# Performance work log

Measured on AMD Instinct MI355X. Metric: run time of the kernel, lower is better.

The kernel has to match this reference:

```python
import jax, jax.numpy as jnp
import numpy as np

D_MODEL = 1024
N_HEAD = 16
HEAD_DIM = D_MODEL // N_HEAD


def setup_inputs() -> dict:
    key = jax.random.key(0)
    k1, k2, k3 = jax.random.split(key, 3)
    B, T = 2, 2048
    x = jax.random.normal(k1, (B, T, D_MODEL), dtype=jnp.float32)
    # nn.MultiheadAttention packed in-projection: (3*D, D), xavier-like scale
    w_in = jax.random.normal(k2, (3 * D_MODEL, D_MODEL), dtype=jnp.float32) * (1.0 / np.sqrt(D_MODEL))
    b_in = jnp.zeros((3 * D_MODEL,), dtype=jnp.float32)
    w_out = jax.random.normal(k3, (D_MODEL, D_MODEL), dtype=jnp.float32) * (1.0 / np.sqrt(D_MODEL))
    b_out = jnp.zeros((D_MODEL,), dtype=jnp.float32)
    return {"x": x, "w_in": w_in, "b_in": b_in, "w_out": w_out, "b_out": b_out}


def reference(x, w_in, b_in, w_out, b_out):
    B, T, D = x.shape
    H, hd = N_HEAD, HEAD_DIM
    # packed QKV projection (torch Linear convention: y = x @ W.T + b)
    qkv = x @ w_in.T + b_in                      # [B, T, 3D]
    q, k, v = jnp.split(qkv, 3, axis=-1)
    # [B, H, T, hd]
    q = q.reshape(B, T, H, hd).transpose(0, 2, 1, 3)
    k = k.reshape(B, T, H, hd).transpose(0, 2, 1, 3)
    v = v.reshape(B, T, H, hd).transpose(0, 2, 1, 3)
    scale = 1.0 / np.sqrt(hd).astype(np.float32)
    scores = jnp.einsum("bhqd,bhkd->bhqk", q * scale, k)  # [B, H, T, T]
    causal = jnp.tril(jnp.ones((T, T), dtype=bool))
    scores = jnp.where(causal, scores, jnp.finfo(scores.dtype).min)
    attn = jax.nn.softmax(scores, axis=-1)
    ctx = jnp.einsum("bhqk,bhkd->bhqd", attn, v)           # [B, H, T, hd]
    ctx = ctx.transpose(0, 2, 1, 3).reshape(B, T, D)
    return ctx @ w_out.T + b_out
```

## Files before the change

kernel.cpp:

```cpp
#include <hip/hip_runtime.h>


#define T_SEQ 2048
#define D_MODEL 1024
#define NEG_BIG (-1.0e30f)

typedef float f32x4 __attribute__((ext_vector_type(4)));
typedef short s16x8 __attribute__((ext_vector_type(8)));
typedef __bf16 bf16x8 __attribute__((ext_vector_type(8)));

__device__ __forceinline__ f32x4 mfma16(s16x8 a, s16x8 b, f32x4 c) {
    return __builtin_amdgcn_mfma_f32_16x16x32_bf16(
        __builtin_bit_cast(bf16x8, a), __builtin_bit_cast(bf16x8, b), c, 0, 0, 0);
}

__device__ __forceinline__ short f2bf(float f) {
    unsigned int u = __float_as_uint(f);
    u += 0x7fffu + ((u >> 16) & 1u);
    return (short)(u >> 16);
}
__device__ __forceinline__ short f2bf_fast(float f) {
    return (short)((__float_as_uint(f) + 0x8000u) >> 16);
}
__device__ __forceinline__ float bf2f(short s) {
    return __uint_as_float(((unsigned int)(unsigned short)s) << 16);
}

__device__ __forceinline__ void async_lds16(const short* g, short* l) {
    __builtin_amdgcn_global_load_lds(
        (const __attribute__((address_space(1))) unsigned int*)g,
        (__attribute__((address_space(3))) unsigned int*)l, 16, 0, 0);
}

#define N_X   4194304
#define N_WI  3145728
#define N_BI  3072
#define N_WO  1048576
#define N_BO  1024
#define V_X   (N_X  / 4)
#define V_WI  (N_WI / 4)
#define V_BI  (N_BI / 4)
#define V_WO  (N_WO / 4)
#define V_BO  (N_BO / 4)
#define V_TOT (V_X + V_WI + V_BI + V_WO + V_BO)

__global__ __launch_bounds__(256) void canon_all_kernel(
    const float* __restrict__ x, const float* __restrict__ wi,
    const float* __restrict__ bi, const float* __restrict__ wo,
    const float* __restrict__ bo,
    short* __restrict__ xb, short* __restrict__ wib, short* __restrict__ bib,
    short* __restrict__ wob, short* __restrict__ bob)
{
    int i = blockIdx.x * 256 + threadIdx.x;
    if (i >= V_TOT) return;
    const float* src; short* dst; int off;
    if      (i < V_X)                    { src = x;  dst = xb;  off = i; }
    else if (i < V_X+V_WI)               { src = wi; dst = wib; off = i - V_X; }
    else if (i < V_X+V_WI+V_BI)          { src = bi; dst = bib; off = i - V_X - V_WI; }
    else if (i < V_X+V_WI+V_BI+V_WO)     { src = wo; dst = wob; off = i - V_X - V_WI - V_BI; }
    else                                 { src = bo; dst = bob; off = i - V_X - V_WI - V_BI - V_WO; }
    float4 v = ((const float4*)src)[off];
    short4 o = { f2bf(v.x), f2bf(v.y), f2bf(v.z), f2bf(v.w) };
    ((short4*)dst)[off] = o;
}

#define Q_SCALE 0.18033688f

__global__ __launch_bounds__(256) void gemm_qkv_kernel(
    const short* __restrict__ A, const short* __restrict__ B,
    const short* __restrict__ bias,
    short* __restrict__ qo, short* __restrict__ ko, short* __restrict__ vo)
{
    const int K = 1024;
    alignas(16) __shared__ short As[128][32];
    alignas(16) __shared__ short Bs[128][32];
    const int m0 = blockIdx.x * 128;
    const int n0 = blockIdx.y * 128;
    const int tid = threadIdx.x;
    const int lane = tid & 63;
    const int w = tid >> 6;
    const int wm = (w >> 1) * 64, wn = (w & 1) * 64;
    const int quad = lane >> 4, l16 = lane & 15;

    f32x4 acc[4][4];
    const f32x4 zero = {0.f, 0.f, 0.f, 0.f};
#pragma unroll
    for (int i = 0; i < 4; ++i)
#pragma unroll
        for (int j = 0; j < 4; ++j) acc[i][j] = zero;

    const int lrow = lane >> 2;
    const int lcol = (lane & 3) * 8;
    const short* gA0 = &A[(m0 + w*32      + lrow) * K + lcol];
    const short* gA1 = &A[(m0 + w*32 + 16 + lrow) * K + lcol];
    const short* gB0 = &B[(n0 + w*32      + lrow) * K + lcol];
    const short* gB1 = &B[(n0 + w*32 + 16 + lrow) * K + lcol];
    short* lA0 = &As[w*32][0];
    short* lA1 = &As[w*32 + 16][0];
    short* lB0 = &Bs[w*32][0];
    short* lB1 = &Bs[w*32 + 16][0];

    for (int k0 = 0; k0 < K; k0 += 32) {
        __syncthreads();
        async_lds16(gA0 + k0, lA0);
        async_lds16(gA1 + k0, lA1);
        async_lds16(gB0 + k0, lB0);
        async_lds16(gB1 + k0, lB1);
        __syncthreads();

        s16x8 af[4], bfr[4];
#pragma unroll
        for (int i = 0; i < 4; ++i) af[i]  = *(const s16x8*)&As[wm + i*16 + l16][quad*8];
#pragma unroll
        for (int j = 0; j < 4; ++j) bfr[j] = *(const s16x8*)&Bs[wn + j*16 + l16][quad*8];
#pragma unroll
        for (int i = 0; i < 4; ++i)
#pragma unroll
            for (int j = 0; j < 4; ++j)
                acc[i][j] = mfma16(af[i], bfr[j], acc[i][j]);
    }

#pragma unroll
    for (int j = 0; j < 4; ++j) {
        int n = n0 + wn + j*16 + l16;
        float bi = bf2f(bias[n]);
        int which = n >> 10;
        short* dst = (which == 0) ? qo : (which == 1) ? ko : vo;
        float scl = (which == 0) ? Q_SCALE : 1.0f;
        int h = (n >> 6) & 15, d = n & 63;
#pragma unroll
        for (int i = 0; i < 4; ++i) {
#pragma unroll
            for (int r = 0; r < 4; ++r) {
                int m = m0 + wm + i*16 + quad*4 + r;
                int b = m >> 11, t = m & 2047;
                float v = (acc[i][j][r] + bi) * scl;
                dst[(((b*16 + h) * 2048) + t) * 64 + d] = f2bf(v);
            }
        }
    }
}

__global__ __launch_bounds__(256) void attn_kernel(
    const short* __restrict__ Q, const short* __restrict__ K,
    const short* __restrict__ V, short* __restrict__ ctx)
{
    alignas(16) __shared__ short Ks[64][72];
    alignas(16) __shared__ short Vt[64][64];
    alignas(16) __shared__ short Pl[4][16][76];

    const int bh = blockIdx.x;
    const int qt = 31 - (int)blockIdx.y;
    const int qbase = qt * 64;
    const int tid = threadIdx.x;
    const int w = tid >> 6, lane = tid & 63;
    const int quad = lane >> 4, l16 = lane & 15;
    const int b = bh >> 4, h = bh & 15;

    const short* Qb = Q + bh * T_SEQ * 64;
    const short* Kb = K + bh * T_SEQ * 64;
    const short* Vb = V + bh * T_SEQ * 64;

    const short* qrow = Qb + (qbase + w*16 + l16) * 64;
    const s16x8 qa0 = *(const s16x8*)(qrow + quad*8);
    const s16x8 qa1 = *(const s16x8*)(qrow + 32 + quad*8);

    const f32x4 zero = {0.f, 0.f, 0.f, 0.f};
    f32x4 o[4];
#pragma unroll
    for (int dt = 0; dt < 4; ++dt) o[dt] = zero;
    float lrow[4] = {0.f, 0.f, 0.f, 0.f};

    const int sr  = tid >> 3;
    const int scl = (tid & 7) * 8;

    for (int s0 = 0; s0 <= qbase; s0 += 64) {
        __syncthreads();
        *(float4*)&Ks[sr][scl]    = *(const float4*)&Kb[(s0 + sr) * 64 + scl];
        *(float4*)&Ks[sr+32][scl] = *(const float4*)&Kb[(s0 + sr + 32) * 64 + scl];
        float4 v0 = *(const float4*)&Vb[(s0 + sr) * 64 + scl];
        float4 v1 = *(const float4*)&Vb[(s0 + sr + 32) * 64 + scl];
        const short* p0 = (const short*)&v0;
        const short* p1 = (const short*)&v1;
#pragma unroll
        for (int j = 0; j < 8; ++j) {
            Vt[scl + j][sr ^ scl]        = p0[j];
            Vt[scl + j][(sr + 32) ^ scl] = p1[j];
        }
        __syncthreads();

        s16x8 kb0[4], kb1[4];
#pragma unroll
        for (int sub = 0; sub < 4; ++sub) {
            kb0[sub] = *(const s16x8*)&Ks[sub*16 + l16][quad*8];
            kb1[sub] = *(const s16x8*)&Ks[sub*16 + l16][32 + quad*8];
        }

        f32x4 S[4];
#pragma unroll
        for (int sub = 0; sub < 4; ++sub)
            S[sub] = mfma16(qa1, kb1[sub], mfma16(qa0, kb0[sub], zero));

        if (s0 == qbase) {
            int q0 = qbase + w*16 + quad*4;
#pragma unroll
            for (int sub = 0; sub < 4; ++sub) {
                int scg = s0 + sub*16 + l16;
#pragma unroll
                for (int r = 0; r < 4; ++r)
                    if (scg > q0 + r) S[sub][r] = NEG_BIG;
            }
        }

        int prow = quad*4;
#pragma unroll
        for (int sub = 0; sub < 4; ++sub) {
#pragma unroll
            for (int r = 0; r < 4; ++r) {
                float p = exp2f(S[sub][r]);
                lrow[r] += p;
                Pl[w][prow + r][sub*16 + l16] = f2bf_fast(p);
            }
        }

        s16x8 pa0 = *(const s16x8*)&Pl[w][l16][quad*8];
        s16x8 pa1 = *(const s16x8*)&Pl[w][l16][32 + quad*8];
#pragma unroll
        for (int dt = 0; dt < 4; ++dt) {
            int e = (dt*2 + (l16 >> 3)) & 7;
            s16x8 vb0 = *(const s16x8*)&Vt[dt*16 + l16][8 * (quad ^ e)];
            s16x8 vb1 = *(const s16x8*)&Vt[dt*16 + l16][8 * ((quad + 4) ^ e)];
            o[dt] = mfma16(pa1, vb1, mfma16(pa0, vb0, o[dt]));
        }
    }

#pragma unroll
    for (int r = 0; r < 4; ++r) {
        float l = lrow[r];
        l += __shfl_xor(l, 1, 16);
        l += __shfl_xor(l, 2, 16);
        l += __shfl_xor(l, 4, 16);
        l += __shfl_xor(l, 8, 16);
        float inv = 1.0f / l;
        int qg = qbase + w*16 + quad*4 + r;
        int base = (b * T_SEQ + qg) * D_MODEL + h * 64 + l16;
#pragma unroll
        for (int dt = 0; dt < 4; ++dt)
            ctx[base + dt*16] = f2bf(o[dt][r] * inv);
    }
}

__global__ __launch_bounds__(256) void gemm_out_kernel(
    const short* __restrict__ A, const short* __restrict__ B,
    const short* __restrict__ bias, float* __restrict__ out)
{
    const int K = 1024;
    alignas(16) __shared__ short As[128][32];
    alignas(16) __shared__ short Bs[128][32];
    const int m0 = blockIdx.x * 128;
    const int n0 = blockIdx.y * 128;
    const int tid = threadIdx.x;
    const int lane = tid & 63;
    const int w = tid >> 6;
    const int wm = (w >> 1) * 64, wn = (w & 1) * 64;
    const int quad = lane >> 4, l16 = lane & 15;

    f32x4 acc[4][4];
    const f32x4 zero = {0.f, 0.f, 0.f, 0.f};
#pragma unroll
    for (int i = 0; i < 4; ++i)
#pragma unroll
        for (int j = 0; j < 4; ++j) acc[i][j] = zero;

    const int lrow = lane >> 2;
    const int lcol = (lane & 3) * 8;
    const short* gA0 = &A[(m0 + w*32      + lrow) * K + lcol];
    const short* gA1 = &A[(m0 + w*32 + 16 + lrow) * K + lcol];
    const short* gB0 = &B[(n0 + w*32      + lrow) * K + lcol];
    const short* gB1 = &B[(n0 + w*32 + 16 + lrow) * K + lcol];
    short* lA0 = &As[w*32][0];
    short* lA1 = &As[w*32 + 16][0];
    short* lB0 = &Bs[w*32][0];
    short* lB1 = &Bs[w*32 + 16][0];

    for (int k0 = 0; k0 < K; k0 += 32) {
        __syncthreads();
        async_lds16(gA0 + k0, lA0);
        async_lds16(gA1 + k0, lA1);
        async_lds16(gB0 + k0, lB0);
        async_lds16(gB1 + k0, lB1);
        __syncthreads();

        s16x8 af[4], bfr[4];
#pragma unroll
        for (int i = 0; i < 4; ++i) af[i]  = *(const s16x8*)&As[wm + i*16 + l16][quad*8];
#pragma unroll
        for (int j = 0; j < 4; ++j) bfr[j] = *(const s16x8*)&Bs[wn + j*16 + l16][quad*8];
#pragma unroll
        for (int i = 0; i < 4; ++i)
#pragma unroll
            for (int j = 0; j < 4; ++j)
                acc[i][j] = mfma16(af[i], bfr[j], acc[i][j]);
    }

#pragma unroll
    for (int j = 0; j < 4; ++j) {
        int n = n0 + wn + j*16 + l16;
        float bi = bf2f(bias[n]);
#pragma unroll
        for (int i = 0; i < 4; ++i) {
#pragma unroll
            for (int r = 0; r < 4; ++r) {
                int m = m0 + wm + i*16 + quad*4 + r;
                out[m * 1024 + n] = acc[i][j][r] + bi;
            }
        }
    }
}

extern "C" void kernel_launch(void* const* d_in, const int* in_sizes, int n_in,
                              void* d_out, int out_size, void* d_ws, size_t ws_size,
                              hipStream_t stream) {
    float* out = (float*)d_out;
    char* ws = (char*)d_ws;

    const size_t MB = 1u << 20;
    short* xb     = (short*)(ws);
    short* w_inb  = (short*)(ws + 8*MB);
    short* b_inb  = (short*)(ws + 14*MB);
    short* w_outb = (short*)(ws + 15*MB);
    short* b_outb = (short*)(ws + 17*MB);
    short* qb     = (short*)(ws + 18*MB);
    short* kb     = (short*)(ws + 26*MB);
    short* vb     = (short*)(ws + 34*MB);
    short* ctxb   = (short*)(ws + 42*MB);

    canon_all_kernel<<<(V_TOT + 255) / 256, 256, 0, stream>>>(
        (const float*)d_in[0], (const float*)d_in[1], (const float*)d_in[2],
        (const float*)d_in[3], (const float*)d_in[4],
        xb, w_inb, b_inb, w_outb, b_outb);

    gemm_qkv_kernel<<<dim3(32, 24), 256, 0, stream>>>(xb, w_inb, b_inb, qb, kb, vb);
    attn_kernel<<<dim3(32, 32), 256, 0, stream>>>(qb, kb, vb, ctxb);
    gemm_out_kernel<<<dim3(32, 8), 256, 0, stream>>>(ctxb, w_outb, b_outb, out);
}
```

Before: 193.6 us.

## Store V transposed from QKV GEMM, swap attention MFMA operands, narrow out-proj tiles

The QKV GEMM now writes V in a transposed [bh][d][t] layout with packed 4-element stores. The attention kernel can then load V tiles into LDS with plain vector copies instead of a scalar transpose-scatter. Attention also swaps the MFMA operands (K·Q and V·P) so each lane owns one query row, which simplifies the row-sum reduction and allows packed P and ctx writes. The output GEMM switches to 128x64 tiles, doubling the grid for better CU occupancy at the cost of more A-tile reloads.

```diff
diff --git a/kernel.cpp b/kernel.cpp
--- a/kernel.cpp
+++ b/kernel.cpp
@@ -4,6 +4,7 @@
 #define T_SEQ 2048
 #define D_MODEL 1024
 #define NEG_BIG (-1.0e30f)
+#define Q_SCALE 0.18033688f
 
 typedef float f32x4 __attribute__((ext_vector_type(4)));
 typedef short s16x8 __attribute__((ext_vector_type(8)));
@@ -19,8 +20,13 @@
     u += 0x7fffu + ((u >> 16) & 1u);
     return (short)(u >> 16);
 }
-__device__ __forceinline__ short f2bf_fast(float f) {
-    return (short)((__float_as_uint(f) + 0x8000u) >> 16);
+__device__ __forceinline__ unsigned f2bfu(float f) {
+    unsigned int u = __float_as_uint(f);
+    u += 0x7fffu + ((u >> 16) & 1u);
+    return u >> 16;
+}
+__device__ __forceinline__ unsigned f2bfu_fast(float f) {
+    return (__float_as_uint(f) + 0x8000u) >> 16;
 }
 __device__ __forceinline__ float bf2f(short s) {
     return __uint_as_float(((unsigned int)(unsigned short)s) << 16);
@@ -64,12 +70,10 @@
     ((short4*)dst)[off] = o;
 }
 
-#define Q_SCALE 0.18033688f
-
 __global__ __launch_bounds__(256) void gemm_qkv_kernel(
     const short* __restrict__ A, const short* __restrict__ B,
     const short* __restrict__ bias,
-    short* __restrict__ qo, short* __restrict__ ko, short* __restrict__ vo)
+    short* __restrict__ qo, short* __restrict__ ko, short* __restrict__ vt)
 {
     const int K = 1024;
     alignas(16) __shared__ short As[128][32];
@@ -125,17 +129,29 @@
         int n = n0 + wn + j*16 + l16;
         float bi = bf2f(bias[n]);
         int which = n >> 10;
-        short* dst = (which == 0) ? qo : (which == 1) ? ko : vo;
-        float scl = (which == 0) ? Q_SCALE : 1.0f;
         int h = (n >> 6) & 15, d = n & 63;
-#pragma unroll
-        for (int i = 0; i < 4; ++i) {
-#pragma unroll
-            for (int r = 0; r < 4; ++r) {
-                int m = m0 + wm + i*16 + quad*4 + r;
-                int b = m >> 11, t = m & 2047;
-                float v = (acc[i][j][r] + bi) * scl;
-                dst[(((b*16 + h) * 2048) + t) * 64 + d] = f2bf(v);
+        if (which == 2) {
+#pragma unroll
+            for (int i = 0; i < 4; ++i) {
+                int tb = m0 + wm + i*16 + quad*4;
+                int b = tb >> 11, t = tb & 2047;
+                uint2 pk;
+                pk.x = f2bfu(acc[i][j][0] + bi) | (f2bfu(acc[i][j][1] + bi) << 16);
+                pk.y = f2bfu(acc[i][j][2] + bi) | (f2bfu(acc[i][j][3] + bi) << 16);
+                *(uint2*)&vt[(((size_t)(b*16 + h)) * 64 + d) * 2048 + t] = pk;
+            }
+        } else {
+            short* dst = (which == 0) ? qo : ko;
+            float scl = (which == 0) ? Q_SCALE : 1.0f;
+#pragma unroll
+            for (int i = 0; i < 4; ++i) {
+#pragma unroll
+                for (int r = 0; r < 4; ++r) {
+                    int m = m0 + wm + i*16 + quad*4 + r;
+                    int b = m >> 11, t = m & 2047;
+                    float v = (acc[i][j][r] + bi) * scl;
+                    dst[(((b*16 + h) * 2048) + t) * 64 + d] = f2bf(v);
+                }
             }
         }
     }
@@ -143,11 +159,11 @@
 
 __global__ __launch_bounds__(256) void attn_kernel(
     const short* __restrict__ Q, const short* __restrict__ K,
-    const short* __restrict__ V, short* __restrict__ ctx)
+    const short* __restrict__ Vt, short* __restrict__ ctx)
 {
     alignas(16) __shared__ short Ks[64][72];
-    alignas(16) __shared__ short Vt[64][64];
-    alignas(16) __shared__ short Pl[4][16][76];
+    alignas(16) __shared__ short Vs[64][72];
+    alignas(16) __shared__ short Pl[4][16][72];
 
     const int bh = blockIdx.x;
     const int qt = 31 - (int)blockIdx.y;
@@ -157,9 +173,9 @@
     const int quad = lane >> 4, l16 = lane & 15;
     const int b = bh >> 4, h = bh & 15;
 
-    const short* Qb = Q + bh * T_SEQ * 64;
-    const short* Kb = K + bh * T_SEQ * 64;
-    const short* Vb = V + bh * T_SEQ * 64;
+    const short* Qb  = Q  + bh * T_SEQ * 64;
+    const short* Kb  = K  + bh * T_SEQ * 64;
+    const short* Vbt = Vt + bh * 64 * T_SEQ;
 
     const short* qrow = Qb + (qbase + w*16 + l16) * 64;
     const s16x8 qa0 = *(const s16x8*)(qrow + quad*8);
@@ -169,84 +185,60 @@
     f32x4 o[4];
 #pragma unroll
     for (int dt = 0; dt < 4; ++dt) o[dt] = zero;
-    float lrow[4] = {0.f, 0.f, 0.f, 0.f};
+    float lsum = 0.f;
 
     const int sr  = tid >> 3;
     const int scl = (tid & 7) * 8;
+    const int qg  = qbase + w*16 + l16;
 
     for (int s0 = 0; s0 <= qbase; s0 += 64) {
         __syncthreads();
         *(float4*)&Ks[sr][scl]    = *(const float4*)&Kb[(s0 + sr) * 64 + scl];
         *(float4*)&Ks[sr+32][scl] = *(const float4*)&Kb[(s0 + sr + 32) * 64 + scl];
-        float4 v0 = *(const float4*)&Vb[(s0 + sr) * 64 + scl];
-        float4 v1 = *(const float4*)&Vb[(s0 + sr + 32) * 64 + scl];
-        const short* p0 = (const short*)&v0;
-        const short* p1 = (const short*)&v1;
-#pragma unroll
-        for (int j = 0; j < 8; ++j) {
-            Vt[scl + j][sr ^ scl]        = p0[j];
-            Vt[scl + j][(sr + 32) ^ scl] = p1[j];
+        *(float4*)&Vs[sr][scl]    = *(const float4*)&Vbt[(size_t)sr * T_SEQ + s0 + scl];
+        *(float4*)&Vs[sr+32][scl] = *(const float4*)&Vbt[(size_t)(sr + 32) * T_SEQ + s0 + scl];
+        __syncthreads();
+
+#pragma unroll
+        for (int sub = 0; sub < 4; ++sub) {
+            s16x8 ka0 = *(const s16x8*)&Ks[sub*16 + l16][quad*8];
+            s16x8 ka1 = *(const s16x8*)&Ks[sub*16 + l16][32 + quad*8];
+            f32x4 S = mfma16(ka1, qa1, mfma16(ka0, qa0, zero));
+            if (s0 == qbase) {
+                int sb = s0 + sub*16 + quad*4;
+#pragma unroll
+                for (int r = 0; r < 4; ++r)
+                    if (sb + r > qg) S[r] = NEG_BIG;
+            }
+            float p0 = exp2f(S[0]), p1 = exp2f(S[1]);
+            float p2 = exp2f(S[2]), p3 = exp2f(S[3]);
+            lsum += (p0 + p1) + (p2 + p3);
+            uint2 pk;
+            pk.x = f2bfu_fast(p0) | (f2bfu_fast(p1) << 16);
+            pk.y = f2bfu_fast(p2) | (f2bfu_fast(p3) << 16);
+            *(uint2*)&Pl[w][l16][sub*16 + quad*4] = pk;
         }
-        __syncthreads();
-
-        s16x8 kb0[4], kb1[4];
-#pragma unroll
-        for (int sub = 0; sub < 4; ++sub) {
-            kb0[sub] = *(const s16x8*)&Ks[sub*16 + l16][quad*8];
-            kb1[sub] = *(const s16x8*)&Ks[sub*16 + l16][32 + quad*8];
+
+        s16x8 pb0 = *(const s16x8*)&Pl[w][l16][quad*8];
+        s16x8 pb1 = *(const s16x8*)&Pl[w][l16][32 + quad*8];
+#pragma unroll
+        for (int dt = 0; dt < 4; ++dt) {
+            s16x8 va0 = *(const s16x8*)&Vs[dt*16 + l16][quad*8];
+            s16x8 va1 = *(const s16x8*)&Vs[dt*16 + l16][32 + quad*8];
+            o[dt] = mfma16(va1, pb1, mfma16(va0, pb0, o[dt]));
         }
-
-        f32x4 S[4];
-#pragma unroll
-        for (int sub = 0; sub < 4; ++sub)
-            S[sub] = mfma16(qa1, kb1[sub], mfma16(qa0, kb0[sub], zero));
-
-        if (s0 == qbase) {
-            int q0 = qbase + w*16 + quad*4;
-#pragma unroll
-            for (int sub = 0; sub < 4; ++sub) {
-                int scg = s0 + sub*16 + l16;
-#pragma unroll
-                for (int r = 0; r < 4; ++r)
-                    if (scg > q0 + r) S[sub][r] = NEG_BIG;
-            }
-        }
-
-        int prow = quad*4;
-#pragma unroll
-        for (int sub = 0; sub < 4; ++sub) {
-#pragma unroll
-            for (int r = 0; r < 4; ++r) {
-                float p = exp2f(S[sub][r]);
-                lrow[r] += p;
-                Pl[w][prow + r][sub*16 + l16] = f2bf_fast(p);
-            }
-        }
-
-        s16x8 pa0 = *(const s16x8*)&Pl[w][l16][quad*8];
-        s16x8 pa1 = *(const s16x8*)&Pl[w][l16][32 + quad*8];
-#pragma unroll
-        for (int dt = 0; dt < 4; ++dt) {
-            int e = (dt*2 + (l16 >> 3)) & 7;
-            s16x8 vb0 = *(const s16x8*)&Vt[dt*16 + l16][8 * (quad ^ e)];
-            s16x8 vb1 = *(const s16x8*)&Vt[dt*16 + l16][8 * ((quad + 4) ^ e)];
-            o[dt] = mfma16(pa1, vb1, mfma16(pa0, vb0, o[dt]));
-        }
-    }
-
-#pragma unroll
-    for (int r = 0; r < 4; ++r) {
-        float l = lrow[r];
-        l += __shfl_xor(l, 1, 16);
-        l += __shfl_xor(l, 2, 16);
-        l += __shfl_xor(l, 4, 16);
-        l += __shfl_xor(l, 8, 16);
-        float inv = 1.0f / l;
-        int qg = qbase + w*16 + quad*4 + r;
-        int base = (b * T_SEQ + qg) * D_MODEL + h * 64 + l16;
-#pragma unroll
-        for (int dt = 0; dt < 4; ++dt)
-            ctx[base + dt*16] = f2bf(o[dt][r] * inv);
+    }
+
+    lsum += __shfl_xor(lsum, 16, 64);
+    lsum += __shfl_xor(lsum, 32, 64);
+    float inv = 1.0f / lsum;
+    int base = (b * T_SEQ + qg) * D_MODEL + h * 64;
+#pragma unroll
+    for (int dt = 0; dt < 4; ++dt) {
+        uint2 pk;
+        pk.x = f2bfu(o[dt][0] * inv) | (f2bfu(o[dt][1] * inv) << 16);
+        pk.y = f2bfu(o[dt][2] * inv) | (f2bfu(o[dt][3] * inv) << 16);
+        *(uint2*)&ctx[base + dt*16 + quad*4] = pk;
     }
 }
 
@@ -256,55 +248,52 @@
 {
     const int K = 1024;
     alignas(16) __shared__ short As[128][32];
-    alignas(16) __shared__ short Bs[128][32];
+    alignas(16) __shared__ short Bs[64][32];
     const int m0 = blockIdx.x * 128;
-    const int n0 = blockIdx.y * 128;
+    const int n0 = blockIdx.y * 64;
     const int tid = threadIdx.x;
     const int lane = tid & 63;
     const int w = tid >> 6;
-    const int wm = (w >> 1) * 64, wn = (w & 1) * 64;
+    const int wm = (w >> 1) * 64, wn = (w & 1) * 32;
     const int quad = lane >> 4, l16 = lane & 15;
 
-    f32x4 acc[4][4];
+    f32x4 acc[4][2];
     const f32x4 zero = {0.f, 0.f, 0.f, 0.f};
 #pragma unroll
     for (int i = 0; i < 4; ++i)
 #pragma unroll
-        for (int j = 0; j < 4; ++j) acc[i][j] = zero;
+        for (int j = 0; j < 2; ++j) acc[i][j] = zero;
 
     const int lrow = lane >> 2;
     const int lcol = (lane & 3) * 8;
     const short* gA0 = &A[(m0 + w*32      + lrow) * K + lcol];
     const short* gA1 = &A[(m0 + w*32 + 16 + lrow) * K + lcol];
-    const short* gB0 = &B[(n0 + w*32      + lrow) * K + lcol];
-    const short* gB1 = &B[(n0 + w*32 + 16 + lrow) * K + lcol];
+    const short* gB0 = &B[(n0 + w*16      + lrow) * K + lcol];
     short* lA0 = &As[w*32][0];
     short* lA1 = &As[w*32 + 16][0];
-    short* lB0 = &Bs[w*32][0];
-    short* lB1 = &Bs[w*32 + 16][0];
+    short* lB0 = &Bs[w*16][0];
 
     for (int k0 = 0; k0 < K; k0 += 32) {
         __syncthreads();
         async_lds16(gA0 + k0, lA0);
         async_lds16(gA1 + k0, lA1);
         async_lds16(gB0 + k0, lB0);
-        async_lds16(gB1 + k0, lB1);
-        __syncthreads();
-
-        s16x8 af[4], bfr[4];
+        __syncthreads();
+
+        s16x8 af[4], bfr[2];
 #pragma unroll
         for (int i = 0; i < 4; ++i) af[i]  = *(const s16x8*)&As[wm + i*16 + l16][quad*8];
 #pragma unroll
-        for (int j = 0; j < 4; ++j) bfr[j] = *(const s16x8*)&Bs[wn + j*16 + l16][quad*8];
+        for (int j = 0; j < 2; ++j) bfr[j] = *(const s16x8*)&Bs[wn + j*16 + l16][quad*8];
 #pragma unroll
         for (int i = 0; i < 4; ++i)
 #pragma unroll
-            for (int j = 0; j < 4; ++j)
+            for (int j = 0; j < 2; ++j)
                 acc[i][j] = mfma16(af[i], bfr[j], acc[i][j]);
     }
 
 #pragma unroll
-    for (int j = 0; j < 4; ++j) {
+    for (int j = 0; j < 2; ++j) {
         int n = n0 + wn + j*16 + l16;
         float bi = bf2f(bias[n]);
 #pragma unroll
@@ -332,7 +321,7 @@
     short* b_outb = (short*)(ws + 17*MB);
     short* qb     = (short*)(ws + 18*MB);
     short* kb     = (short*)(ws + 26*MB);
-    short* vb     = (short*)(ws + 34*MB);
+    short* vtb    = (short*)(ws + 34*MB);
     short* ctxb   = (short*)(ws + 42*MB);
 
     canon_all_kernel<<<(V_TOT + 255) / 256, 256, 0, stream>>>(
@@ -340,7 +329,7 @@
         (const float*)d_in[3], (const float*)d_in[4],
         xb, w_inb, b_inb, w_outb, b_outb);
 
-    gemm_qkv_kernel<<<dim3(32, 24), 256, 0, stream>>>(xb, w_inb, b_inb, qb, kb, vb);
-    attn_kernel<<<dim3(32, 32), 256, 0, stream>>>(qb, kb, vb, ctxb);
-    gemm_out_kernel<<<dim3(32, 8), 256, 0, stream>>>(ctxb, w_outb, b_outb, out);
-}
+    gemm_qkv_kernel<<<dim3(32, 24), 256, 0, stream>>>(xb, w_inb, b_inb, qb, kb, vtb);
+    attn_kernel<<<dim3(32, 32), 256, 0, stream>>>(qb, kb, vtb, ctxb);
+    gemm_out_kernel<<<dim3(32, 16), 256, 0, stream>>>(ctxb, w_outb, b_outb, out);
+}
```

Measured after the change: 195.8 us. Within noise of the previous version (+1.1%).
